# Optimization experiments

Hardware: AMD Instinct MI355X
Metric: run time of the kernel (lower is better)

The kernel has to match this reference:

```python
import jax, jax.numpy as jnp
import numpy as np

H = 64      # num query heads
HKV = 8     # num key/value heads
D = 64      # head_dim
HID = 2880  # hidden_size
B = 8       # batch (num sequences)
Q = 16      # query tokens per sequence
P = 128     # kv pages per sequence
PAGE = 16   # kv page size
NPAGES = 2048  # total pages in cache pool
NEG = -1e9  # finite stand-in for -inf mask (avoids inf arithmetic; exp underflows to 0 identically)


def setup_inputs() -> dict:
    key = jax.random.key(0)
    ks = jax.random.split(key, 6)
    n = B * Q
    S = P * PAGE
    hidden_states = jax.random.normal(ks[0], (n, HID), jnp.float32) * 0.02
    kv_cache_at_layer = jax.random.normal(ks[1], (NPAGES, 2, PAGE, HKV, D), jnp.float32)
    qkv_dim = D * (H + 2 * HKV)
    w_qkv = jax.random.normal(ks[2], (qkv_dim, HID), jnp.float32) * 0.02
    b_qkv = jnp.zeros((qkv_dim,), jnp.float32)
    w_o = jax.random.normal(ks[3], (HID, H * D), jnp.float32) * 0.02
    b_o = jnp.zeros((HID,), jnp.float32)
    sinks = jax.random.normal(ks[4], (H,), jnp.float32)
    qo_indptr = (jnp.arange(B + 1) * Q).astype(jnp.int32)
    kv_page_indptr = (jnp.arange(B + 1) * P).astype(jnp.int32)
    kv_last_page_lens = jnp.full((B,), PAGE, jnp.int32)
    kv_page_indices = jnp.asarray(np.random.default_rng(0).permutation(NPAGES)[:B * P], jnp.int32)
    # causal mask: query i of each sequence sits at absolute position S - Q + i
    qpos = S - Q + jnp.arange(Q)
    mask = jnp.where(jnp.arange(S)[None, :] <= qpos[:, None], 0.0, NEG).astype(jnp.float32)
    attention_mask = jnp.broadcast_to(mask[None], (B, Q, S)).reshape(-1)
    return dict(hidden_states=hidden_states, kv_cache_at_layer=kv_cache_at_layer,
                attention_mask=attention_mask, w_qkv=w_qkv, b_qkv=b_qkv, w_o=w_o, b_o=b_o,
                sinks=sinks, qo_indptr=qo_indptr, kv_page_indptr=kv_page_indptr,
                kv_last_page_lens=kv_last_page_lens, kv_page_indices=kv_page_indices)


def reference(hidden_states, kv_cache_at_layer, attention_mask, w_qkv, b_qkv, w_o, b_o,
              sinks, qo_indptr, kv_page_indptr, kv_last_page_lens, kv_page_indices):
    n = hidden_states.shape[0]
    b = qo_indptr.shape[0] - 1
    q_len = n // b                              # uniform ragged layout (see setup)
    p = kv_page_indices.shape[0] // b
    page = kv_cache_at_layer.shape[2]
    s = p * page
    g = H // HKV                                # query heads per kv head (GQA groups)
    scaling = D ** -0.5

    qkv = hidden_states @ w_qkv.T + b_qkv                       # [n, (H+2*HKV)*D]
    q = qkv[:, :H * D].reshape(b, q_len, HKV, g, D) * scaling    # [b q hkv g d]

    pages = kv_page_indices.reshape(b, p)
    k = kv_cache_at_layer[pages, 0].reshape(b, s, HKV, D)        # gather pages -> [b s hkv d]
    v = kv_cache_at_layer[pages, 1].reshape(b, s, HKV, D)

    scores = jnp.einsum('bqhgd,bshd->bhgqs', q, k).astype(jnp.float32)
    mask = attention_mask.reshape(b, q_len, s)
    # keys beyond the valid portion of the last page are invalid
    valid = jnp.arange(s)[None, :] < ((p - 1) * page + kv_last_page_lens[:, None])
    mask = jnp.where(valid[:, None, :], mask, NEG)
    scores = scores + mask[:, None, None, :, :]

    # online-softmax merge across pages is equivalent to this single pass;
    # running max starts at 0 in the original, hence the clamp to 0
    m = jnp.maximum(scores.max(axis=-1), 0.0)                    # [b hkv g q]
    pexp = jnp.exp(scores - m[..., None])                        # [b hkv g q s]
    sink = sinks.reshape(HKV, g).astype(jnp.float32)
    sum_exp = pexp.sum(axis=-1) + jnp.exp(sink[None, :, :, None] - m)
    num = jnp.einsum('bhgqs,bshd->bhgqd', pexp, v.astype(jnp.float32))
    attn = num / sum_exp[..., None]                              # [b hkv g q d]
    attn = attn.transpose(0, 3, 1, 2, 4).reshape(n, H * D)       # q (h d)
    return attn.astype(hidden_states.dtype) @ w_o.T + b_o
```

## Files before the change

kernel.cpp:

```cpp
#include <hip/hip_runtime.h>
#include <hip/hip_bf16.h>

#define BB      8
#define QL      16
#define NHKV    8
#define NG      8
#define DD      64
#define HIDN    2880
#define PP      128
#define PGSZ    16
#define SS      2048
#define NQ      4096
#define NSPLIT  8
#define KSQ     5
#define KCQ     576
#define KSO     8
#define KCO     512

typedef short bf16x8 __attribute__((ext_vector_type(8)));
typedef short short4v __attribute__((ext_vector_type(4)));
typedef float f32x4  __attribute__((ext_vector_type(4)));

__device__ inline short f2bf(float f) {
  __hip_bfloat16 h = __float2bfloat16(f);
  union { __hip_bfloat16 h; short s; } u; u.h = h;
  return u.s;
}

__device__ inline float bf2f(short s) {
  union { float f; unsigned u; } u;
  u.u = ((unsigned)(unsigned short)s) << 16;
  return u.f;
}

__device__ inline bf16x8 cvt8(float4 a, float4 b) {
  bf16x8 r;
  r[0] = f2bf(a.x); r[1] = f2bf(a.y); r[2] = f2bf(a.z); r[3] = f2bf(a.w);
  r[4] = f2bf(b.x); r[5] = f2bf(b.y); r[6] = f2bf(b.z); r[7] = f2bf(b.w);
  return r;
}

__device__ inline bf16x8 pack8(const float* __restrict__ p) {
  float4 a = *(const float4*)p;
  float4 b = *(const float4*)(p + 4);
  return cvt8(a, b);
}

__global__ __launch_bounds__(256) void k_qkv_split(const float* __restrict__ hid,
                                                   const float* __restrict__ wq,
                                                   short* __restrict__ qpart) {
  const int n0 = blockIdx.x * 32;
  const int ks = blockIdx.y;
  const int tid = threadIdx.x;
  const int wid = tid >> 6, lane = tid & 63;
  const int lo = lane & 15, hi = lane >> 4;
  const int m0 = wid * 32;

  const float* xr0 = hid + (size_t)(m0 + lo) * HIDN;
  const float* xr1 = hid + (size_t)(m0 + 16 + lo) * HIDN;
  const float* wr0 = wq + (size_t)(n0 + lo) * HIDN;
  const float* wr1 = wq + (size_t)(n0 + 16 + lo) * HIDN;
  const int kb = ks * KCQ + hi * 8;

  f32x4 acc[2][2];
#pragma unroll
  for (int mt = 0; mt < 2; ++mt)
#pragma unroll
    for (int nt = 0; nt < 2; ++nt) acc[mt][nt] = (f32x4){0.f, 0.f, 0.f, 0.f};

  float4 bufA[4][2], bufB[4][2];
#define LOADQ(dst, kk) { \
    dst[0][0] = *(const float4*)(xr0 + (kk));     dst[0][1] = *(const float4*)(xr0 + (kk) + 4); \
    dst[1][0] = *(const float4*)(xr1 + (kk));     dst[1][1] = *(const float4*)(xr1 + (kk) + 4); \
    dst[2][0] = *(const float4*)(wr0 + (kk));     dst[2][1] = *(const float4*)(wr0 + (kk) + 4); \
    dst[3][0] = *(const float4*)(wr1 + (kk));     dst[3][1] = *(const float4*)(wr1 + (kk) + 4); }
#define MFMAQ(buf) { \
    bf16x8 a0 = cvt8(buf[0][0], buf[0][1]); \
    bf16x8 a1 = cvt8(buf[1][0], buf[1][1]); \
    bf16x8 w0 = cvt8(buf[2][0], buf[2][1]); \
    bf16x8 w1 = cvt8(buf[3][0], buf[3][1]); \
    acc[0][0] = __builtin_amdgcn_mfma_f32_16x16x32_bf16(a0, w0, acc[0][0], 0, 0, 0); \
    acc[0][1] = __builtin_amdgcn_mfma_f32_16x16x32_bf16(a0, w1, acc[0][1], 0, 0, 0); \
    acc[1][0] = __builtin_amdgcn_mfma_f32_16x16x32_bf16(a1, w0, acc[1][0], 0, 0, 0); \
    acc[1][1] = __builtin_amdgcn_mfma_f32_16x16x32_bf16(a1, w1, acc[1][1], 0, 0, 0); }

  LOADQ(bufA, kb);
#pragma unroll
  for (int it = 0; it < 9; ++it) {
    const int kk = kb + it * 64;
    LOADQ(bufB, kk + 32);
    MFMAQ(bufA);
    if (it < 8) LOADQ(bufA, kk + 64);
    MFMAQ(bufB);
  }
#undef LOADQ
#undef MFMAQ

  short* qp = qpart + (size_t)ks * 128 * NQ;
#pragma unroll
  for (int mt = 0; mt < 2; ++mt)
#pragma unroll
    for (int nt = 0; nt < 2; ++nt)
#pragma unroll
      for (int r = 0; r < 4; ++r) {
        int m = m0 + mt * 16 + hi * 4 + r;
        int n = n0 + nt * 16 + lo;
        qp[(size_t)m * NQ + n] = f2bf(acc[mt][nt][r]);
      }
}

__global__ __launch_bounds__(256) void k_attn(const float* __restrict__ kvc,
                                              const int* __restrict__ pidx,
                                              const int* __restrict__ llen,
                                              const short* __restrict__ qpart,
                                              const float* __restrict__ bq,
                                              short* __restrict__ opart,
                                              float* __restrict__ lbuf) {
  const int blk = blockIdx.x;
  const int pair = blk >> 3, split = blk & 7;
  const int b = pair >> 3, kvh = pair & 7;
  const int tid = threadIdx.x;
  const int wid = tid >> 6, lane = tid & 63;
  const int lo = lane & 15, hi = lane >> 4;
  const int wrow = wid * 32;

  __shared__ short plds[128][72];
  __shared__ float vlds[64][65];

  bf16x8 qf[2][2];
#pragma unroll
  for (int mt = 0; mt < 2; ++mt) {
    int r = wrow + mt * 16 + lo;
    int g = r >> 4, qq = r & 15;
    int m = b * QL + qq;
    int h = kvh * NG + g;
#pragma unroll
    for (int kg = 0; kg < 2; ++kg) {
      int n = h * DD + kg * 32 + hi * 8;
      float4 b0 = *(const float4*)(bq + n);
      float4 b1 = *(const float4*)(bq + n + 4);
      float s[8];
      s[0] = b0.x; s[1] = b0.y; s[2] = b0.z; s[3] = b0.w;
      s[4] = b1.x; s[5] = b1.y; s[6] = b1.z; s[7] = b1.w;
#pragma unroll
      for (int k2 = 0; k2 < KSQ; ++k2) {
        bf16x8 p = *(const bf16x8*)(qpart + ((size_t)k2 * 128 + m) * NQ + n);
#pragma unroll
        for (int j = 0; j < 8; ++j) s[j] += bf2f(p[j]);
      }
      bf16x8 q8;
#pragma unroll
      for (int j = 0; j < 8; ++j) q8[j] = f2bf(s[j] * 0.125f);
      qf[mt][kg] = q8;
    }
  }

  float l_part[2][4];
  f32x4 o_acc[2][4];
#pragma unroll
  for (int mt = 0; mt < 2; ++mt)
#pragma unroll
    for (int j = 0; j < 4; ++j) l_part[mt][j] = 0.f;
#pragma unroll
  for (int mt = 0; mt < 2; ++mt)
#pragma unroll
    for (int dt = 0; dt < 4; ++dt) o_acc[mt][dt] = (f32x4){0.f, 0.f, 0.f, 0.f};

  const int sKeepEnd = (PP - 1) * PGSZ + llen[b];
  const int* pib = pidx + b * PP;
  const int sBeg = split * (SS / NSPLIT);
  const int sEnd = sBeg + (SS / NSPLIT);

  for (int s0 = sBeg; s0 < sEnd; s0 += 64) {
    float4 vreg[4];
    const int vsr = tid >> 4;
    const int vc4 = (tid & 15) * 4;
#pragma unroll
    for (int pc = 0; pc < 4; ++pc) {
      int pg = pib[(s0 >> 4) + pc];
      vreg[pc] = *(const float4*)(kvc +
          ((((size_t)pg * 2 + 1) * PGSZ + vsr) * NHKV + kvh) * DD + vc4);
    }

    f32x4 sc[2][4];
#pragma unroll
    for (int mt = 0; mt < 2; ++mt)
#pragma unroll
      for (int nt = 0; nt < 4; ++nt) sc[mt][nt] = (f32x4){0.f, 0.f, 0.f, 0.f};

#pragma unroll
    for (int nt = 0; nt < 4; ++nt) {
      int s = s0 + nt * 16 + lo;
      int pg = pib[s >> 4];
      const float* kp = kvc + ((((size_t)pg * 2 + 0) * PGSZ + (s & 15)) * NHKV + kvh) * DD;
#pragma unroll
      for (int kg = 0; kg < 2; ++kg) {
        bf16x8 kf = pack8(kp + kg * 32 + hi * 8);
        sc[0][nt] = __builtin_amdgcn_mfma_f32_16x16x32_bf16(qf[0][kg], kf, sc[0][nt], 0, 0, 0);
        sc[1][nt] = __builtin_amdgcn_mfma_f32_16x16x32_bf16(qf[1][kg], kf, sc[1][nt], 0, 0, 0);
      }
    }

    if (s0 + 64 > SS - QL) {
#pragma unroll
      for (int mt = 0; mt < 2; ++mt)
#pragma unroll
        for (int j = 0; j < 4; ++j) {
          int r = wrow + mt * 16 + hi * 4 + j;
          int qq = r & 15;
          int sLimQ = (SS - QL) + qq;
#pragma unroll
          for (int nt = 0; nt < 4; ++nt) {
            int s = s0 + nt * 16 + lo;
            bool keep = (s <= sLimQ) && (s < sKeepEnd);
            sc[mt][nt][j] = keep ? sc[mt][nt][j] : -1.0e9f;
          }
        }
    }

#pragma unroll
    for (int mt = 0; mt < 2; ++mt)
#pragma unroll
      for (int j = 0; j < 4; ++j)
#pragma unroll
        for (int nt = 0; nt < 4; ++nt) {
          float p = __expf(sc[mt][nt][j]);
          sc[mt][nt][j] = p;
          l_part[mt][j] += p;
        }

    __syncthreads();
#pragma unroll
    for (int pc = 0; pc < 4; ++pc) {
      int sl = pc * 16 + vsr;
      vlds[sl][vc4]     = vreg[pc].x;
      vlds[sl][vc4 + 1] = vreg[pc].y;
      vlds[sl][vc4 + 2] = vreg[pc].z;
      vlds[sl][vc4 + 3] = vreg[pc].w;
    }
#pragma unroll
    for (int mt = 0; mt < 2; ++mt)
#pragma unroll
      for (int j = 0; j < 4; ++j) {
        int r = wrow + mt * 16 + hi * 4 + j;
#pragma unroll
        for (int nt = 0; nt < 4; ++nt)
          plds[r][nt * 16 + lo] = f2bf(sc[mt][nt][j]);
      }
    __syncthreads();

#pragma unroll
    for (int kg = 0; kg < 2; ++kg) {
      bf16x8 pa[2];
      pa[0] = *(const bf16x8*)(&plds[wrow + lo][kg * 32 + hi * 8]);
      pa[1] = *(const bf16x8*)(&plds[wrow + 16 + lo][kg * 32 + hi * 8]);
#pragma unroll
      for (int dt = 0; dt < 4; ++dt) {
        bf16x8 vf;
#pragma unroll
        for (int j = 0; j < 8; ++j)
          vf[j] = f2bf(vlds[kg * 32 + hi * 8 + j][dt * 16 + lo]);
        o_acc[0][dt] = __builtin_amdgcn_mfma_f32_16x16x32_bf16(pa[0], vf, o_acc[0][dt], 0, 0, 0);
        o_acc[1][dt] = __builtin_amdgcn_mfma_f32_16x16x32_bf16(pa[1], vf, o_acc[1][dt], 0, 0, 0);
      }
    }
  }

#pragma unroll
  for (int mt = 0; mt < 2; ++mt)
#pragma unroll
    for (int j = 0; j < 4; ++j)
#pragma unroll
      for (int off = 1; off < 16; off <<= 1)
        l_part[mt][j] += __shfl_xor(l_part[mt][j], off, 64);

  short* op = opart + (size_t)(pair * NSPLIT + split) * 128 * DD;
#pragma unroll
  for (int mt = 0; mt < 2; ++mt)
#pragma unroll
    for (int dt = 0; dt < 4; ++dt)
#pragma unroll
      for (int j = 0; j < 4; ++j) {
        int r = wrow + mt * 16 + hi * 4 + j;
        op[r * DD + dt * 16 + lo] = f2bf(o_acc[mt][dt][j]);
      }
  if (lo == 0) {
#pragma unroll
    for (int mt = 0; mt < 2; ++mt)
#pragma unroll
      for (int j = 0; j < 4; ++j) {
        int r = wrow + mt * 16 + hi * 4 + j;
        lbuf[(size_t)(pair * NSPLIT + split) * 128 + r] = l_part[mt][j];
      }
  }
}

__global__ __launch_bounds__(256) void k_merge(const short* __restrict__ opart,
                                               const float* __restrict__ lbuf,
                                               const float* __restrict__ sinks,
                                               short* __restrict__ attnbf) {
  const int pair = blockIdx.x;
  const int b = pair >> 3, kvh = pair & 7;
  const int tid = threadIdx.x;

  __shared__ float Ls[128];
  if (tid < 128) {
    int r = tid, g = r >> 4;
    float L = __expf(sinks[kvh * NG + g]);
#pragma unroll
    for (int s2 = 0; s2 < NSPLIT; ++s2)
      L += lbuf[(size_t)(pair * NSPLIT + s2) * 128 + r];
    Ls[r] = L;
  }
  __syncthreads();

  for (int u = tid; u < 128 * 16; u += 256) {
    int r = u >> 4, c4 = (u & 15) * 4;
    float o0 = 0.f, o1 = 0.f, o2 = 0.f, o3 = 0.f;
#pragma unroll
    for (int s2 = 0; s2 < NSPLIT; ++s2) {
      short4v pv = *(const short4v*)(opart +
          ((size_t)(pair * NSPLIT + s2) * 128 + r) * DD + c4);
      o0 += bf2f(pv[0]); o1 += bf2f(pv[1]); o2 += bf2f(pv[2]); o3 += bf2f(pv[3]);
    }
    float inv = 1.0f / Ls[r];
    int g = r >> 4, qq = r & 15;
    int h = kvh * NG + g;
    short4v ov;
    ov[0] = f2bf(o0 * inv); ov[1] = f2bf(o1 * inv);
    ov[2] = f2bf(o2 * inv); ov[3] = f2bf(o3 * inv);
    *(short4v*)(attnbf + (size_t)(b * QL + qq) * NQ + h * DD + c4) = ov;
  }
}

__global__ __launch_bounds__(256) void k_out_split(const short* __restrict__ attnbf,
                                                   const float* __restrict__ wo,
                                                   short* __restrict__ outpart) {
  const int n0 = blockIdx.x * 32;
  const int ks = blockIdx.y;
  const int tid = threadIdx.x;
  const int wid = tid >> 6, lane = tid & 63;
  const int lo = lane & 15, hi = lane >> 4;
  const int m0 = wid * 32;

  const short* ar0 = attnbf + (size_t)(m0 + lo) * NQ;
  const short* ar1 = attnbf + (size_t)(m0 + 16 + lo) * NQ;
  const float* wr0 = wo + (size_t)(n0 + lo) * NQ;
  const float* wr1 = wo + (size_t)(n0 + 16 + lo) * NQ;
  const int kb = ks * KCO + hi * 8;

  f32x4 acc[2][2];
#pragma unroll
  for (int mt = 0; mt < 2; ++mt)
#pragma unroll
    for (int nt = 0; nt < 2; ++nt) acc[mt][nt] = (f32x4){0.f, 0.f, 0.f, 0.f};

  bf16x8 aA[2], aB[2];
  float4 wA[2][2], wB[2][2];
#define LOADO(adst, wdst, kk) { \
    adst[0] = *(const bf16x8*)(ar0 + (kk)); \
    adst[1] = *(const bf16x8*)(ar1 + (kk)); \
    wdst[0][0] = *(const float4*)(wr0 + (kk)); wdst[0][1] = *(const float4*)(wr0 + (kk) + 4); \
    wdst[1][0] = *(const float4*)(wr1 + (kk)); wdst[1][1] = *(const float4*)(wr1 + (kk) + 4); }
#define MFMAO(abuf, wbuf) { \
    bf16x8 w0 = cvt8(wbuf[0][0], wbuf[0][1]); \
    bf16x8 w1 = cvt8(wbuf[1][0], wbuf[1][1]); \
    acc[0][0] = __builtin_amdgcn_mfma_f32_16x16x32_bf16(abuf[0], w0, acc[0][0], 0, 0, 0); \
    acc[0][1] = __builtin_amdgcn_mfma_f32_16x16x32_bf16(abuf[0], w1, acc[0][1], 0, 0, 0); \
    acc[1][0] = __builtin_amdgcn_mfma_f32_16x16x32_bf16(abuf[1], w0, acc[1][0], 0, 0, 0); \
    acc[1][1] = __builtin_amdgcn_mfma_f32_16x16x32_bf16(abuf[1], w1, acc[1][1], 0, 0, 0); }

  LOADO(aA, wA, kb);
#pragma unroll
  for (int it = 0; it < 8; ++it) {
    const int kk = kb + it * 64;
    LOADO(aB, wB, kk + 32);
    MFMAO(aA, wA);
    if (it < 7) LOADO(aA, wA, kk + 64);
    MFMAO(aB, wB);
  }
#undef LOADO
#undef MFMAO

  short* op = outpart + (size_t)ks * 128 * HIDN;
#pragma unroll
  for (int mt = 0; mt < 2; ++mt)
#pragma unroll
    for (int nt = 0; nt < 2; ++nt)
#pragma unroll
      for (int r = 0; r < 4; ++r) {
        int m = m0 + mt * 16 + hi * 4 + r;
        int n = n0 + nt * 16 + lo;
        op[(size_t)m * HIDN + n] = f2bf(acc[mt][nt][r]);
      }
}

__global__ __launch_bounds__(256) void k_ored(const short* __restrict__ outpart,
                                              const float* __restrict__ bo,
                                              float* __restrict__ out) {
  int idx = blockIdx.x * 256 + threadIdx.x;
  int m = idx / 720;
  int n = (idx - m * 720) * 4;
  float4 v = *(const float4*)(bo + n);
#pragma unroll
  for (int ks = 0; ks < KSO; ++ks) {
    short4v p = *(const short4v*)(outpart + ((size_t)ks * 128 + m) * HIDN + n);
    v.x += bf2f(p[0]); v.y += bf2f(p[1]); v.z += bf2f(p[2]); v.w += bf2f(p[3]);
  }
  *(float4*)(out + (size_t)m * HIDN + n) = v;
}

extern "C" void kernel_launch(void* const* d_in, const int* in_sizes, int n_in,
                              void* d_out, int out_size, void* d_ws, size_t ws_size,
                              hipStream_t stream) {
  const float* hid   = (const float*)d_in[0];
  const float* kvc   = (const float*)d_in[1];
  const float* wq    = (const float*)d_in[3];
  const float* bq    = (const float*)d_in[4];
  const float* wo    = (const float*)d_in[5];
  const float* bo    = (const float*)d_in[6];
  const float* sinks = (const float*)d_in[7];
  const int* llen    = (const int*)d_in[10];
  const int* pidx    = (const int*)d_in[11];
  float* out = (float*)d_out;

  char* ws = (char*)d_ws;
  short* qpart   = (short*)(ws + 0);
  short* attnbf  = (short*)(ws + 5242880);
  short* opart   = (short*)(ws + 6291456);
  float* lbuf    = (float*)(ws + 14680064);
  short* outpart = (short*)(ws + 14942208);

  k_qkv_split<<<dim3(128, KSQ), dim3(256), 0, stream>>>(hid, wq, qpart);
  k_attn<<<dim3(BB * NHKV * NSPLIT), dim3(256), 0, stream>>>(kvc, pidx, llen, qpart, bq, opart, lbuf);
  k_merge<<<dim3(BB * NHKV), dim3(256), 0, stream>>>(opart, lbuf, sinks, attnbf);
  k_out_split<<<dim3(HIDN / 32, KSO), dim3(256), 0, stream>>>(attnbf, wo, outpart);
  k_ored<<<dim3(360), dim3(256), 0, stream>>>(outpart, bo, out);
}
```

Baseline: 127.9 us.

## Double split-K and attention splits, triple-buffer GEMM loads, transpose V in LDS

Doubles the split-K factor of both projection GEMMs and the KV split count of attention, and splits the merge kernel into quarters, so every stage launches more blocks. The GEMM inner loops move from double to triple buffering of global loads. In attention, V is converted to bf16 and stored transposed in LDS, so each MFMA operand becomes one vector read instead of eight scalar float reads and conversions. In exchange, more partial sums are written and reduced, and the workspace grows.

New measurement: 150.0 us. +17.3%, slower.

```diff
diff --git a/kernel.cpp b/kernel.cpp
--- a/kernel.cpp
+++ b/kernel.cpp
@@ -11,11 +11,11 @@
 #define PGSZ    16
 #define SS      2048
 #define NQ      4096
-#define NSPLIT  8
-#define KSQ     5
-#define KCQ     576
-#define KSO     8
-#define KCO     512
+#define NSPLIT  16
+#define KSQ     10
+#define KCQ     288
+#define KSO     16
+#define KCO     256
 
 typedef short bf16x8 __attribute__((ext_vector_type(8)));
 typedef short short4v __attribute__((ext_vector_type(4)));
@@ -68,12 +68,12 @@
 #pragma unroll
     for (int nt = 0; nt < 2; ++nt) acc[mt][nt] = (f32x4){0.f, 0.f, 0.f, 0.f};
 
-  float4 bufA[4][2], bufB[4][2];
+  float4 b0[4][2], b1[4][2], b2[4][2];
 #define LOADQ(dst, kk) { \
-    dst[0][0] = *(const float4*)(xr0 + (kk));     dst[0][1] = *(const float4*)(xr0 + (kk) + 4); \
-    dst[1][0] = *(const float4*)(xr1 + (kk));     dst[1][1] = *(const float4*)(xr1 + (kk) + 4); \
-    dst[2][0] = *(const float4*)(wr0 + (kk));     dst[2][1] = *(const float4*)(wr0 + (kk) + 4); \
-    dst[3][0] = *(const float4*)(wr1 + (kk));     dst[3][1] = *(const float4*)(wr1 + (kk) + 4); }
+    dst[0][0] = *(const float4*)(xr0 + (kk)); dst[0][1] = *(const float4*)(xr0 + (kk) + 4); \
+    dst[1][0] = *(const float4*)(xr1 + (kk)); dst[1][1] = *(const float4*)(xr1 + (kk) + 4); \
+    dst[2][0] = *(const float4*)(wr0 + (kk)); dst[2][1] = *(const float4*)(wr0 + (kk) + 4); \
+    dst[3][0] = *(const float4*)(wr1 + (kk)); dst[3][1] = *(const float4*)(wr1 + (kk) + 4); }
 #define MFMAQ(buf) { \
     bf16x8 a0 = cvt8(buf[0][0], buf[0][1]); \
     bf16x8 a1 = cvt8(buf[1][0], buf[1][1]); \
@@ -84,15 +84,16 @@
     acc[1][0] = __builtin_amdgcn_mfma_f32_16x16x32_bf16(a1, w0, acc[1][0], 0, 0, 0); \
     acc[1][1] = __builtin_amdgcn_mfma_f32_16x16x32_bf16(a1, w1, acc[1][1], 0, 0, 0); }
 
-  LOADQ(bufA, kb);
-#pragma unroll
-  for (int it = 0; it < 9; ++it) {
-    const int kk = kb + it * 64;
-    LOADQ(bufB, kk + 32);
-    MFMAQ(bufA);
-    if (it < 8) LOADQ(bufA, kk + 64);
-    MFMAQ(bufB);
-  }
+  LOADQ(b0, kb);        LOADQ(b1, kb + 32);
+  LOADQ(b2, kb + 64);   MFMAQ(b0);
+  LOADQ(b0, kb + 96);   MFMAQ(b1);
+  LOADQ(b1, kb + 128);  MFMAQ(b2);
+  LOADQ(b2, kb + 160);  MFMAQ(b0);
+  LOADQ(b0, kb + 192);  MFMAQ(b1);
+  LOADQ(b1, kb + 224);  MFMAQ(b2);
+  LOADQ(b2, kb + 256);  MFMAQ(b0);
+  MFMAQ(b1);
+  MFMAQ(b2);
 #undef LOADQ
 #undef MFMAQ
 
@@ -117,7 +118,7 @@
                                               short* __restrict__ opart,
                                               float* __restrict__ lbuf) {
   const int blk = blockIdx.x;
-  const int pair = blk >> 3, split = blk & 7;
+  const int pair = blk >> 4, split = blk & 15;
   const int b = pair >> 3, kvh = pair & 7;
   const int tid = threadIdx.x;
   const int wid = tid >> 6, lane = tid & 63;
@@ -125,7 +126,7 @@
   const int wrow = wid * 32;
 
   __shared__ short plds[128][72];
-  __shared__ float vlds[64][65];
+  __shared__ short vtlds[64][72];
 
   bf16x8 qf[2][2];
 #pragma unroll
@@ -137,11 +138,11 @@
 #pragma unroll
     for (int kg = 0; kg < 2; ++kg) {
       int n = h * DD + kg * 32 + hi * 8;
-      float4 b0 = *(const float4*)(bq + n);
-      float4 b1 = *(const float4*)(bq + n + 4);
+      float4 bb0 = *(const float4*)(bq + n);
+      float4 bb1 = *(const float4*)(bq + n + 4);
       float s[8];
-      s[0] = b0.x; s[1] = b0.y; s[2] = b0.z; s[3] = b0.w;
-      s[4] = b1.x; s[5] = b1.y; s[6] = b1.z; s[7] = b1.w;
+      s[0] = bb0.x; s[1] = bb0.y; s[2] = bb0.z; s[3] = bb0.w;
+      s[4] = bb1.x; s[5] = bb1.y; s[6] = bb1.z; s[7] = bb1.w;
 #pragma unroll
       for (int k2 = 0; k2 < KSQ; ++k2) {
         bf16x8 p = *(const bf16x8*)(qpart + ((size_t)k2 * 128 + m) * NQ + n);
@@ -233,10 +234,10 @@
 #pragma unroll
     for (int pc = 0; pc < 4; ++pc) {
       int sl = pc * 16 + vsr;
-      vlds[sl][vc4]     = vreg[pc].x;
-      vlds[sl][vc4 + 1] = vreg[pc].y;
-      vlds[sl][vc4 + 2] = vreg[pc].z;
-      vlds[sl][vc4 + 3] = vreg[pc].w;
+      vtlds[vc4    ][sl] = f2bf(vreg[pc].x);
+      vtlds[vc4 + 1][sl] = f2bf(vreg[pc].y);
+      vtlds[vc4 + 2][sl] = f2bf(vreg[pc].z);
+      vtlds[vc4 + 3][sl] = f2bf(vreg[pc].w);
     }
 #pragma unroll
     for (int mt = 0; mt < 2; ++mt)
@@ -256,10 +257,7 @@
       pa[1] = *(const bf16x8*)(&plds[wrow + 16 + lo][kg * 32 + hi * 8]);
 #pragma unroll
       for (int dt = 0; dt < 4; ++dt) {
-        bf16x8 vf;
-#pragma unroll
-        for (int j = 0; j < 8; ++j)
-          vf[j] = f2bf(vlds[kg * 32 + hi * 8 + j][dt * 16 + lo]);
+        bf16x8 vf = *(const bf16x8*)(&vtlds[dt * 16 + lo][kg * 32 + hi * 8]);
         o_acc[0][dt] = __builtin_amdgcn_mfma_f32_16x16x32_bf16(pa[0], vf, o_acc[0][dt], 0, 0, 0);
         o_acc[1][dt] = __builtin_amdgcn_mfma_f32_16x16x32_bf16(pa[1], vf, o_acc[1][dt], 0, 0, 0);
       }
@@ -299,7 +297,7 @@
                                                const float* __restrict__ lbuf,
                                                const float* __restrict__ sinks,
                                                short* __restrict__ attnbf) {
-  const int pair = blockIdx.x;
+  const int pair = blockIdx.x >> 2, quarter = blockIdx.x & 3;
   const int b = pair >> 3, kvh = pair & 7;
   const int tid = threadIdx.x;
 
@@ -314,8 +312,8 @@
   }
   __syncthreads();
 
-  for (int u = tid; u < 128 * 16; u += 256) {
-    int r = u >> 4, c4 = (u & 15) * 4;
+  for (int u = tid; u < 128 * 4; u += 256) {
+    int r = u >> 2, c4 = (quarter * 4 + (u & 3)) * 4;
     float o0 = 0.f, o1 = 0.f, o2 = 0.f, o3 = 0.f;
 #pragma unroll
     for (int s2 = 0; s2 < NSPLIT; ++s2) {
@@ -355,30 +353,30 @@
 #pragma unroll
     for (int nt = 0; nt < 2; ++nt) acc[mt][nt] = (f32x4){0.f, 0.f, 0.f, 0.f};
 
-  bf16x8 aA[2], aB[2];
-  float4 wA[2][2], wB[2][2];
+  bf16x8 a0[2], a1[2], a2[2];
+  float4 w0[2][2], w1[2][2], w2[2][2];
 #define LOADO(adst, wdst, kk) { \
     adst[0] = *(const bf16x8*)(ar0 + (kk)); \
     adst[1] = *(const bf16x8*)(ar1 + (kk)); \
     wdst[0][0] = *(const float4*)(wr0 + (kk)); wdst[0][1] = *(const float4*)(wr0 + (kk) + 4); \
     wdst[1][0] = *(const float4*)(wr1 + (kk)); wdst[1][1] = *(const float4*)(wr1 + (kk) + 4); }
 #define MFMAO(abuf, wbuf) { \
-    bf16x8 w0 = cvt8(wbuf[0][0], wbuf[0][1]); \
-    bf16x8 w1 = cvt8(wbuf[1][0], wbuf[1][1]); \
-    acc[0][0] = __builtin_amdgcn_mfma_f32_16x16x32_bf16(abuf[0], w0, acc[0][0], 0, 0, 0); \
-    acc[0][1] = __builtin_amdgcn_mfma_f32_16x16x32_bf16(abuf[0], w1, acc[0][1], 0, 0, 0); \
-    acc[1][0] = __builtin_amdgcn_mfma_f32_16x16x32_bf16(abuf[1], w0, acc[1][0], 0, 0, 0); \
-    acc[1][1] = __builtin_amdgcn_mfma_f32_16x16x32_bf16(abuf[1], w1, acc[1][1], 0, 0, 0); }
-
-  LOADO(aA, wA, kb);
-#pragma unroll
-  for (int it = 0; it < 8; ++it) {
-    const int kk = kb + it * 64;
-    LOADO(aB, wB, kk + 32);
-    MFMAO(aA, wA);
-    if (it < 7) LOADO(aA, wA, kk + 64);
-    MFMAO(aB, wB);
-  }
+    bf16x8 ww0 = cvt8(wbuf[0][0], wbuf[0][1]); \
+    bf16x8 ww1 = cvt8(wbuf[1][0], wbuf[1][1]); \
+    acc[0][0] = __builtin_amdgcn_mfma_f32_16x16x32_bf16(abuf[0], ww0, acc[0][0], 0, 0, 0); \
+    acc[0][1] = __builtin_amdgcn_mfma_f32_16x16x32_bf16(abuf[0], ww1, acc[0][1], 0, 0, 0); \
+    acc[1][0] = __builtin_amdgcn_mfma_f32_16x16x32_bf16(abuf[1], ww0, acc[1][0], 0, 0, 0); \
+    acc[1][1] = __builtin_amdgcn_mfma_f32_16x16x32_bf16(abuf[1], ww1, acc[1][1], 0, 0, 0); }
+
+  LOADO(a0, w0, kb);        LOADO(a1, w1, kb + 32);
+  LOADO(a2, w2, kb + 64);   MFMAO(a0, w0);
+  LOADO(a0, w0, kb + 96);   MFMAO(a1, w1);
+  LOADO(a1, w1, kb + 128);  MFMAO(a2, w2);
+  LOADO(a2, w2, kb + 160);  MFMAO(a0, w0);
+  LOADO(a0, w0, kb + 192);  MFMAO(a1, w1);
+  LOADO(a1, w1, kb + 224);  MFMAO(a2, w2);
+  MFMAO(a0, w0);
+  MFMAO(a1, w1);
 #undef LOADO
 #undef MFMAO
 
@@ -426,14 +424,14 @@
 
   char* ws = (char*)d_ws;
   short* qpart   = (short*)(ws + 0);
-  short* attnbf  = (short*)(ws + 5242880);
-  short* opart   = (short*)(ws + 6291456);
-  float* lbuf    = (float*)(ws + 14680064);
-  short* outpart = (short*)(ws + 14942208);
+  short* attnbf  = (short*)(ws + 10485760);
+  short* opart   = (short*)(ws + 11534336);
+  float* lbuf    = (float*)(ws + 28311552);
+  short* outpart = (short*)(ws + 28835840);
 
   k_qkv_split<<<dim3(128, KSQ), dim3(256), 0, stream>>>(hid, wq, qpart);
   k_attn<<<dim3(BB * NHKV * NSPLIT), dim3(256), 0, stream>>>(kvc, pidx, llen, qpart, bq, opart, lbuf);
-  k_merge<<<dim3(BB * NHKV), dim3(256), 0, stream>>>(opart, lbuf, sinks, attnbf);
+  k_merge<<<dim3(BB * NHKV * 4), dim3(256), 0, stream>>>(opart, lbuf, sinks, attnbf);
   k_out_split<<<dim3(HIDN / 32, KSO), dim3(256), 0, stream>>>(attnbf, wo, outpart);
   k_ored<<<dim3(360), dim3(256), 0, stream>>>(outpart, bo, out);
 }
```
